# Optimization experiments

Hardware: AMD Instinct MI355X
Metric: run time of the kernel (lower is better)

The kernel has to match this reference:

```python
import jax, jax.numpy as jnp
import numpy as np

NUM_HEADS = 16
THETA = 10000.0


def _rope(x, cos, sin):
    # x: [B, H, S, d_k]; cos/sin: [S, d_k//2] broadcast over B, H
    x1 = x[..., 0::2]
    x2 = x[..., 1::2]
    r1 = cos * x1 - sin * x2
    r2 = sin * x1 + cos * x2
    # interleave back: (..., half_d, 2) -> (..., d_k)
    return jnp.stack((r1, r2), axis=-1).reshape(x.shape)


def setup_inputs() -> dict:
    key = jax.random.key(0)
    ks = jax.random.split(key, 5)
    B, S, D = 4, 2048, 1024
    scale = D ** -0.5
    x = jax.random.normal(ks[0], (B, S, D), dtype=jnp.float32)
    wq = jax.random.normal(ks[1], (D, D), dtype=jnp.float32) * scale
    wk = jax.random.normal(ks[2], (D, D), dtype=jnp.float32) * scale
    wv = jax.random.normal(ks[3], (D, D), dtype=jnp.float32) * scale
    wo = jax.random.normal(ks[4], (D, D), dtype=jnp.float32) * scale
    return {"x": x, "wq": wq, "wk": wk, "wv": wv, "wo": wo}


def reference(x, wq, wk, wv, wo):
    B, S, D = x.shape
    H = NUM_HEADS
    dk = D // H

    def proj(w):
        # x @ w.T, split heads -> [B, H, S, dk]
        y = jnp.einsum('bsd,ed->bse', x, w)
        return y.reshape(B, S, H, dk).transpose(0, 2, 1, 3)

    q, k, v = proj(wq), proj(wk), proj(wv)

    # RoPE (interleaved pairs), positions = arange(S)
    inv_freq = THETA ** (-(jnp.arange(0, dk, 2, dtype=jnp.float32) / dk))
    ang = jnp.arange(S, dtype=jnp.float32)[:, None] * inv_freq  # [S, dk//2]
    cos, sin = jnp.cos(ang), jnp.sin(ang)
    q = _rope(q, cos, sin)
    k = _rope(k, cos, sin)

    scores = jnp.einsum('bhqd,bhkd->bhqk', q, k) / jnp.sqrt(jnp.asarray(dk, x.dtype))
    causal = jnp.tril(jnp.ones((S, S), dtype=bool))  # keep self + past
    scores = jnp.where(causal, scores, -jnp.inf)
    p = jax.nn.softmax(scores, axis=-1)
    attn = jnp.einsum('bhqk,bhkd->bhqd', p, v)
    attn = attn.transpose(0, 2, 1, 3).reshape(B, S, D)
    return jnp.einsum('bsd,ed->bse', attn, wo)
```

## Files before the change

### kernel.cpp

```cpp
#include <hip/hip_runtime.h>
#include <hip/hip_bf16.h>
#include <cstdint>
#include <cstddef>

#define Bb 4
#define Ss 2048
#define Dd 1024
#define Hh 16
#define Mm (Bb*Ss)

typedef __bf16 bf16_t;
typedef __bf16 bf16x8 __attribute__((ext_vector_type(8)));
typedef __bf16 bf16x4 __attribute__((ext_vector_type(4)));
typedef float  f32x4  __attribute__((ext_vector_type(4)));
typedef float  f32x16 __attribute__((ext_vector_type(16)));
typedef unsigned int u32x4 __attribute__((ext_vector_type(4)));
typedef unsigned int u32x2 __attribute__((ext_vector_type(2)));

#define MFMA16(a,b,c) __builtin_amdgcn_mfma_f32_16x16x32_bf16(a,b,c,0,0,0)
#define MFMA32(a,b,c) __builtin_amdgcn_mfma_f32_32x32x16_bf16(a,b,c,0,0,0)

#define QSCALE 0.18033688011112042f

static __device__ __forceinline__ float fexp2(float x) {
#if __has_builtin(__builtin_amdgcn_exp2f)
  return __builtin_amdgcn_exp2f(x);
#else
  return exp2f(x);
#endif
}

static __device__ __forceinline__ bf16x8 ld16g(const bf16_t* p) {
  return __builtin_bit_cast(bf16x8, *reinterpret_cast<const u32x4*>(p));
}

static __device__ __forceinline__ void gload_lds16(const bf16_t* g, bf16_t* l) {
  __builtin_amdgcn_global_load_lds(
      (__attribute__((address_space(1))) void*)(g),
      (__attribute__((address_space(3))) void*)(l),
      16, 0, 0);
}

__global__ void prep_k(const float* __restrict__ x,  const float* __restrict__ wq,
                       const float* __restrict__ wk, const float* __restrict__ wv,
                       const float* __restrict__ wo,
                       bf16_t* __restrict__ xb, bf16_t* __restrict__ wqkv,
                       float2* __restrict__ tab) {
  int bid = blockIdx.x;
  if (bid < 8192) {
    int i = (bid * 256 + threadIdx.x) * 4;
    float4 f = *reinterpret_cast<const float4*>(x + i);
    xb[i + 0] = (bf16_t)f.x; xb[i + 1] = (bf16_t)f.y;
    xb[i + 2] = (bf16_t)f.z; xb[i + 3] = (bf16_t)f.w;
  } else if (bid < 12288) {
    int b2 = bid - 8192;
    int seg = b2 >> 10, local = b2 & 1023;
    const float* w = (seg == 0) ? wq : (seg == 1) ? wk : (seg == 2) ? wv : wo;
    int i = (local * 256 + threadIdx.x) * 4;
    float4 f = *reinterpret_cast<const float4*>(w + i);
    bf16_t* o = wqkv + (size_t)seg * (Dd * Dd) + i;
    o[0] = (bf16_t)f.x; o[1] = (bf16_t)f.y; o[2] = (bf16_t)f.z; o[3] = (bf16_t)f.w;
  } else {
    int idx = (bid - 12288) * 256 + threadIdx.x;
    int i = idx & 31, s = idx >> 5;
    float inv_freq = exp2f(-(float)i * (13.2877123795494f / 32.0f));
    float ang = (float)s * inv_freq;
    float sn, cs;
    sincosf(ang, &sn, &cs);
    tab[idx] = make_float2(cs, sn);
  }
}

template <typename OutT>
__global__ __launch_bounds__(256, 3) void gemm_r3(const bf16_t* __restrict__ A,
                                                  const bf16_t* __restrict__ Bm,
                                                  OutT* __restrict__ C0,
                                                  OutT* __restrict__ C1,
                                                  bf16_t* __restrict__ VtOut,
                                                  const float2* __restrict__ tab,
                                                  int Kdim) {
  __shared__ bf16_t As[3][128 * 32];
  __shared__ bf16_t Bs[3][128 * 32];
  const int t = threadIdx.x;
  const int lane = t & 63, w = t >> 6;
  const int l15 = lane & 15, lg = lane >> 4;
  const int wr = w >> 1, wc = w & 1;
  const int m0 = blockIdx.x * 128, n0 = blockIdx.y * 128;

  const bf16_t* gA[2];
  const bf16_t* gB[2];
#pragma unroll
  for (int i = 0; i < 2; ++i) {
    int q = i * 256 + t, row = q >> 2, sl = (q & 3) ^ ((row >> 1) & 3);
    gA[i] = A  + (size_t)(m0 + row) * Kdim + sl * 8;
    gB[i] = Bm + (size_t)(n0 + row) * Kdim + sl * 8;
  }
  const int wb = w * 64 * 8;

  auto stage = [&](int slot, int k0) {
#pragma unroll
    for (int i = 0; i < 2; ++i) {
      gload_lds16(gA[i] + k0, &As[slot][i * 2048 + wb]);
      gload_lds16(gB[i] + k0, &Bs[slot][i * 2048 + wb]);
    }
  };

  int aoff[4], boff[4];
#pragma unroll
  for (int i = 0; i < 4; ++i) {
    int row = wr * 64 + i * 16 + l15;
    aoff[i] = row * 32 + ((lg ^ ((row >> 1) & 3)) * 8);
  }
#pragma unroll
  for (int j = 0; j < 4; ++j) {
    int row = wc * 64 + j * 16 + l15;
    boff[j] = row * 32 + ((lg ^ ((row >> 1) & 3)) * 8);
  }

  f32x4 acc[4][4] = {};
  const int KT = Kdim / 32;

  stage(0, 0);
  stage(1, 32);
  for (int j = 0; j < KT; ++j) {
    if (j == KT - 1) {
      asm volatile("s_waitcnt vmcnt(0) lgkmcnt(0)" ::: "memory");
    } else {
      asm volatile("s_waitcnt vmcnt(4) lgkmcnt(0)" ::: "memory");
    }
    __builtin_amdgcn_s_barrier();
    if (j + 2 < KT) stage((j + 2) % 3, (j + 2) * 32);
    const bf16_t* ab = As[j % 3];
    const bf16_t* bb = Bs[j % 3];
    bf16x8 a[4], b[4];
#pragma unroll
    for (int jj = 0; jj < 4; ++jj)
      b[jj] = __builtin_bit_cast(bf16x8,
               *reinterpret_cast<const u32x4*>(bb + boff[jj]));
#pragma unroll
    for (int i = 0; i < 4; ++i)
      a[i] = __builtin_bit_cast(bf16x8,
               *reinterpret_cast<const u32x4*>(ab + aoff[i]));
    __builtin_amdgcn_s_setprio(1);
#pragma unroll
    for (int i = 0; i < 4; ++i)
#pragma unroll
      for (int jj = 0; jj < 4; ++jj)
        acc[i][jj] = MFMA16(a[i], b[jj], acc[i][jj]);
    __builtin_amdgcn_s_setprio(0);
  }

  const int nb = n0 & 1023;
  if (VtOut != nullptr && n0 >= 2048) {
#pragma unroll
    for (int i = 0; i < 4; ++i) {
      int rowb = m0 + wr * 64 + i * 16 + lg * 4;
      int b = rowb >> 11, s = rowb & 2047;
#pragma unroll
      for (int j = 0; j < 4; ++j) {
        int col = nb + wc * 64 + j * 16 + l15;
        int h = col >> 6, d = col & 63;
        bf16x4 ov;
#pragma unroll
        for (int r = 0; r < 4; ++r) ov[r] = (bf16_t)acc[i][j][r];
        *reinterpret_cast<u32x2*>(
            &VtOut[(((size_t)(b * 16 + h)) * 64 + d) * 2048 + s]) =
            __builtin_bit_cast(u32x2, ov);
      }
    }
    return;
  }
  OutT* Cs = (n0 < 1024) ? C0 : C1;
  const bool doRope = (tab != nullptr) && (n0 < 2048);
  const float qs = (n0 < 1024) ? QSCALE : 1.0f;

  if (doRope) {
#pragma unroll
    for (int i = 0; i < 4; ++i) {
      int rowb = m0 + wr * 64 + i * 16 + lg * 4;
#pragma unroll
      for (int j = 0; j < 4; ++j) {
        int col = nb + wc * 64 + j * 16 + l15;
        int i0 = (col & 63) >> 1;
        const bool ev = !(col & 1);
#pragma unroll
        for (int r = 0; r < 4; ++r) {
          float v = acc[i][j][r];
          float px = __shfl_xor(v, 1);
          int s = (rowb + r) & (Ss - 1);
          float2 f = tab[s * 32 + i0];
          float sn = ev ? -f.y : f.y;
          Cs[(size_t)(rowb + r) * 1024 + col] = (OutT)((f.x * v + sn * px) * qs);
        }
      }
    }
  } else {
#pragma unroll
    for (int i = 0; i < 4; ++i) {
      int rowb = m0 + wr * 64 + i * 16 + lg * 4;
#pragma unroll
      for (int j = 0; j < 4; ++j) {
        int col = nb + wc * 64 + j * 16 + l15;
#pragma unroll
        for (int r = 0; r < 4; ++r)
          Cs[(size_t)(rowb + r) * 1024 + col] = (OutT)acc[i][j][r];
      }
    }
  }
}

__global__ __launch_bounds__(256, 2) void attn_k(const bf16_t* __restrict__ Q,
                                                 const bf16_t* __restrict__ K,
                                                 const bf16_t* __restrict__ Vt,
                                                 bf16_t* __restrict__ O) {
  __shared__ bf16_t Ks[2][8192];
  __shared__ bf16_t Vs[2][8192];
  const int t = threadIdx.x, lane = t & 63, w = t >> 6;
  const int l31 = lane & 31, hi = lane >> 5, hi8 = hi * 8;
  const int bh = blockIdx.y, b = bh >> 4, h = bh & 15;
  const int bx = blockIdx.x;
  const int i = bx * 4 + w;
  const int q0a = 32 * i, q0b = 2016 - 32 * i;
  const int dtA = q0a >> 6, hfA = (q0a >> 5) & 1;
  const int dtB = q0b >> 6, hfB = (q0b >> 5) & 1;
  const int NT2 = 16 - bx;
  const bf16_t* qb = Q + (size_t)b * Ss * Dd + h * 64;
  const bf16_t* kb = K + (size_t)b * Ss * Dd + h * 64;
  const bf16_t* vtb = Vt + (size_t)bh * 64 * Ss;

  const int a_ = l31 >> 2, c_ = l31 & 3;
  const int tau = (a_ >> 1) + 2 * (a_ & 1) + ((a_ & 4) >> 1);
  const int sig = c_ + 4 * tau;

  int kfoff[4];
#pragma unroll
  for (int c = 0; c < 4; ++c) {
    int j = sig >> 1, u = (sig & 1) * 8 + c * 2 + hi;
    kfoff[c] = j * 128 + ((u ^ j) * 8);
  }
  int vfoff[2][2];
#pragma unroll
  for (int db = 0; db < 2; ++db)
#pragma unroll
    for (int ks = 0; ks < 2; ++ks) {
      int d = db * 32 + l31, j = d >> 2, u = (d & 3) * 4 + ks * 2 + hi;
      vfoff[db][ks] = j * 128 + ((u ^ j) * 8);
    }

  const int sj = t >> 4, ss = t & 15, su = ss ^ sj;
  const bf16_t* ksrc0 = kb + (size_t)(2 * sj + (su >> 3)) * Dd + (su & 7) * 8;
  const bf16_t* vsrc0 = vtb + (size_t)(4 * sj + (su >> 2)) * Ss + (su & 3) * 8;

  auto stage128 = [&](int buf, int kb0) {
    bf16_t* kd = &Ks[buf][w * 512];
    bf16_t* vd = &Vs[buf][w * 512];
#pragma unroll
    for (int st = 0; st < 4; ++st) {
      gload_lds16(ksrc0 + (size_t)(kb0 + 32 * st) * Dd, kd + st * 2048);
      gload_lds16(vsrc0 + kb0 + 32 * st,                vd + st * 2048);
    }
  };

  bf16x8 qf[2][4];
#pragma unroll
  for (int c = 0; c < 4; ++c) {
    qf[0][c] = ld16g(qb + (size_t)(q0a + l31) * Dd + c * 16 + hi8);
    qf[1][c] = ld16g(qb + (size_t)(q0b + l31) * Dd + c * 16 + hi8);
  }

  float l_[2] = {0.f, 0.f};
  f32x16 o_[2][2] = {};

  auto chain = [&](int kt, int dt, int hf, bf16x8 (&qc)[4],
                   f32x16& o0, f32x16& o1, float& lc,
                   bf16x8 (&kf)[2][4], bf16x8 (&vf)[2][2][2]) {
    if (kt > dt) return;
    const bool last = (kt == dt);
    const bool do1 = !(last && hf == 0);
    f32x16 s0 = {}, s1 = {};
    __builtin_amdgcn_s_setprio(1);
    s0 = MFMA32(kf[0][0], qc[0], s0);
    s0 = MFMA32(kf[0][1], qc[1], s0);
    s0 = MFMA32(kf[0][2], qc[2], s0);
    s0 = MFMA32(kf[0][3], qc[3], s0);
    if (do1) {
      s1 = MFMA32(kf[1][0], qc[0], s1);
      s1 = MFMA32(kf[1][1], qc[1], s1);
      s1 = MFMA32(kf[1][2], qc[2], s1);
      s1 = MFMA32(kf[1][3], qc[3], s1);
    }
    __builtin_amdgcn_s_setprio(0);
    if (last) {
      if (hf) {
#pragma unroll
        for (int reg = 0; reg < 16; ++reg) {
          const int koff = (reg & 3) + 4 * (reg >> 2) + 8 * ((reg >> 2) >> 1) + hi8;
          s1[reg] = (koff <= l31) ? s1[reg] : -INFINITY;
        }
      } else {
#pragma unroll
        for (int reg = 0; reg < 16; ++reg) {
          const int koff = (reg & 3) + 4 * (reg >> 2) + 8 * ((reg >> 2) >> 1) + hi8;
          s0[reg] = (koff <= l31) ? s0[reg] : -INFINITY;
        }
      }
    }
    float p0[16], p1[16];
#pragma unroll
    for (int r = 0; r < 16; ++r) p0[r] = fexp2(s0[r]);
    bf16x8 pa0, pa1, pb0, pb1;
#pragma unroll
    for (int r = 0; r < 8; ++r) { pa0[r] = (bf16_t)p0[r]; pa1[r] = (bf16_t)p0[r + 8]; }
    if (do1) {
#pragma unroll
      for (int r = 0; r < 16; ++r) p1[r] = fexp2(s1[r]);
#pragma unroll
      for (int r = 0; r < 8; ++r) { pb0[r] = (bf16_t)p1[r]; pb1[r] = (bf16_t)p1[r + 8]; }
#pragma unroll
      for (int r = 0; r < 16; ++r) p0[r] += p1[r];
    }
#pragma unroll
    for (int st2 = 8; st2 > 0; st2 >>= 1)
#pragma unroll
      for (int r = 0; r < st2; ++r) p0[r] += p0[r + st2];
    lc += p0[0];
    __builtin_amdgcn_s_setprio(1);
    o0 = MFMA32(vf[0][0][0], pa0, o0);
    o0 = MFMA32(vf[0][0][1], pa1, o0);
    o1 = MFMA32(vf[0][1][0], pa0, o1);
    o1 = MFMA32(vf[0][1][1], pa1, o1);
    if (do1) {
      o0 = MFMA32(vf[1][0][0], pb0, o0);
      o0 = MFMA32(vf[1][0][1], pb1, o0);
      o1 = MFMA32(vf[1][1][0], pb0, o1);
      o1 = MFMA32(vf[1][1][1], pb1, o1);
    }
    __builtin_amdgcn_s_setprio(0);
  };

  stage128(0, 0);
  for (int jj = 0; jj < NT2; ++jj) {
    asm volatile("s_waitcnt vmcnt(0) lgkmcnt(0)" ::: "memory");
    __builtin_amdgcn_s_barrier();
    if (jj + 1 < NT2) stage128((jj + 1) & 1, (jj + 1) * 128);
    const bf16_t* kbuf = &Ks[jj & 1][0];
    const bf16_t* vbuf = &Vs[jj & 1][0];
#pragma unroll
    for (int half = 0; half < 2; ++half) {
      const int kt = 2 * jj + half;
      const int base = half * 4096;
      bf16x8 kf[2][4], vf[2][2][2];
#pragma unroll
      for (int st = 0; st < 2; ++st)
#pragma unroll
        for (int c = 0; c < 4; ++c)
          kf[st][c] = __builtin_bit_cast(bf16x8,
              *reinterpret_cast<const u32x4*>(kbuf + base + st * 2048 + kfoff[c]));
#pragma unroll
      for (int st = 0; st < 2; ++st)
#pragma unroll
        for (int db = 0; db < 2; ++db)
#pragma unroll
          for (int ks = 0; ks < 2; ++ks)
            vf[st][db][ks] = __builtin_bit_cast(bf16x8,
                *reinterpret_cast<const u32x4*>(vbuf + base + st * 2048 + vfoff[db][ks]));
      chain(kt, dtA, hfA, qf[0], o_[0][0], o_[0][1], l_[0], kf, vf);
      chain(kt, dtB, hfB, qf[1], o_[1][0], o_[1][1], l_[1], kf, vf);
    }
  }

#pragma unroll
  for (int ch = 0; ch < 2; ++ch) {
    const float ltot = l_[ch] + __shfl_xor(l_[ch], 32);
    const float inv = 1.0f / ltot;
    const size_t rowoff = ((size_t)b * Ss + (ch ? q0b : q0a) + l31) * Dd + h * 64;
#pragma unroll
    for (int db = 0; db < 2; ++db)
#pragma unroll
      for (int tt = 0; tt < 4; ++tt) {
        bf16x4 ov;
#pragma unroll
        for (int c = 0; c < 4; ++c) ov[c] = (bf16_t)(o_[ch][db][4 * tt + c] * inv);
        *reinterpret_cast<u32x2*>(&O[rowoff + db * 32 + 8 * tt + 4 * hi]) =
            __builtin_bit_cast(u32x2, ov);
      }
  }
}

extern "C" void kernel_launch(void* const* d_in, const int* in_sizes, int n_in,
                              void* d_out, int out_size, void* d_ws, size_t ws_size,
                              hipStream_t stream) {
  (void)in_sizes; (void)n_in; (void)out_size; (void)ws_size;
  const float* x  = (const float*)d_in[0];
  const float* wq = (const float*)d_in[1];
  const float* wk = (const float*)d_in[2];
  const float* wv = (const float*)d_in[3];
  const float* wo = (const float*)d_in[4];
  float* out = (float*)d_out;

  char* ws = (char*)d_ws;
  const size_t MB16 = 16u << 20;
  bf16_t* xb   = (bf16_t*)(ws + 0);
  bf16_t* Qb   = (bf16_t*)(ws + 1 * MB16);
  bf16_t* Kb   = (bf16_t*)(ws + 2 * MB16);
  bf16_t* Vt   = (bf16_t*)(ws + 3 * MB16);
  bf16_t* wqkv = (bf16_t*)(ws + 4 * MB16);
  bf16_t* wob  = wqkv + 3u * Dd * Dd;
  float2* tab  = (float2*)(ws + 4 * MB16 + (8u << 20));
  bf16_t* AOb  = xb;

  prep_k<<<12544, 256, 0, stream>>>(x, wq, wk, wv, wo, xb, wqkv, tab);

  gemm_r3<bf16_t><<<dim3(Mm / 128, 24), 256, 0, stream>>>(xb, wqkv, Qb, Kb, Vt,
                                                          tab, Dd);

  attn_k<<<dim3(8, Bb * Hh), 256, 0, stream>>>(Qb, Kb, Vt, AOb);

  gemm_r3<float><<<dim3(Mm / 128, 8), 256, 0, stream>>>(AOb, wob, out, out,
                                                        nullptr, nullptr, Dd);
}
```

Before: 164.8 us.

## Use 256x256 tile, 1024-thread GEMM for fused QKV projection

Adds a new QKV projection kernel that uses 256x256 output tiles, 16 waves per block, and double-buffered LDS staging, replacing the 128x128 triple-buffered kernel for that GEMM. The larger tile raises arithmetic intensity and cuts global reloads of A and B across the grid. In exchange there are fewer blocks (384), a shallower pipeline, and a full barrier every K step across 16 waves, which could hurt latency hiding and occupancy. The old kernel is specialized to the fp32 output projection only, with the RoPE and Vt epilogues removed.

New measurement: 175.1 us. 6.2% more time.

```diff
diff --git a/kernel.cpp b/kernel.cpp
--- a/kernel.cpp
+++ b/kernel.cpp
@@ -71,13 +71,117 @@
   }
 }
 
-template <typename OutT>
+__global__ __launch_bounds__(1024, 4) void gemm_big(const bf16_t* __restrict__ A,
+                                                    const bf16_t* __restrict__ Bm,
+                                                    bf16_t* __restrict__ C0,
+                                                    bf16_t* __restrict__ C1,
+                                                    bf16_t* __restrict__ VtOut,
+                                                    const float2* __restrict__ tab,
+                                                    int Kdim) {
+  __shared__ bf16_t As[2][256 * 32];
+  __shared__ bf16_t Bs[2][256 * 32];
+  const int t = threadIdx.x;
+  const int lane = t & 63, w = t >> 6;
+  const int l15 = lane & 15, lg = lane >> 4;
+  const int wm = w >> 2, wn = w & 3;
+  const int m0 = blockIdx.x * 256, n0 = blockIdx.y * 256;
+
+  const int row_ = t >> 2, sl_ = (t & 3) ^ ((row_ >> 1) & 3);
+  const bf16_t* gA = A  + (size_t)(m0 + row_) * Kdim + sl_ * 8;
+  const bf16_t* gB = Bm + (size_t)(n0 + row_) * Kdim + sl_ * 8;
+  const int wb = w * 512;
+
+  auto stage = [&](int buf, int k0) {
+    gload_lds16(gA + k0, &As[buf][wb]);
+    gload_lds16(gB + k0, &Bs[buf][wb]);
+  };
+
+  int aoff[4], boff[4];
+#pragma unroll
+  for (int i = 0; i < 4; ++i) {
+    int row = wm * 64 + i * 16 + l15;
+    aoff[i] = row * 32 + ((lg ^ ((row >> 1) & 3)) * 8);
+  }
+#pragma unroll
+  for (int j = 0; j < 4; ++j) {
+    int row = wn * 64 + j * 16 + l15;
+    boff[j] = row * 32 + ((lg ^ ((row >> 1) & 3)) * 8);
+  }
+
+  f32x4 acc[4][4] = {};
+  const int KT = Kdim / 32;
+
+  stage(0, 0);
+  for (int j = 0; j < KT; ++j) {
+    asm volatile("s_waitcnt vmcnt(0) lgkmcnt(0)" ::: "memory");
+    __builtin_amdgcn_s_barrier();
+    if (j + 1 < KT) stage((j + 1) & 1, (j + 1) * 32);
+    const bf16_t* ab = As[j & 1];
+    const bf16_t* bb = Bs[j & 1];
+    bf16x8 a[4], b[4];
+#pragma unroll
+    for (int jj = 0; jj < 4; ++jj)
+      b[jj] = __builtin_bit_cast(bf16x8,
+               *reinterpret_cast<const u32x4*>(bb + boff[jj]));
+#pragma unroll
+    for (int i = 0; i < 4; ++i)
+      a[i] = __builtin_bit_cast(bf16x8,
+               *reinterpret_cast<const u32x4*>(ab + aoff[i]));
+    __builtin_amdgcn_s_setprio(1);
+#pragma unroll
+    for (int i = 0; i < 4; ++i)
+#pragma unroll
+      for (int jj = 0; jj < 4; ++jj)
+        acc[i][jj] = MFMA16(a[i], b[jj], acc[i][jj]);
+    __builtin_amdgcn_s_setprio(0);
+  }
+
+  const int nb = n0 & 1023;
+  if (VtOut != nullptr && n0 >= 2048) {
+#pragma unroll
+    for (int i = 0; i < 4; ++i) {
+      int rowb = m0 + wm * 64 + i * 16 + lg * 4;
+      int b = rowb >> 11, s = rowb & 2047;
+#pragma unroll
+      for (int j = 0; j < 4; ++j) {
+        int col = nb + wn * 64 + j * 16 + l15;
+        int h = col >> 6, d = col & 63;
+        bf16x4 ov;
+#pragma unroll
+        for (int r = 0; r < 4; ++r) ov[r] = (bf16_t)acc[i][j][r];
+        *reinterpret_cast<u32x2*>(
+            &VtOut[(((size_t)(b * 16 + h)) * 64 + d) * 2048 + s]) =
+            __builtin_bit_cast(u32x2, ov);
+      }
+    }
+    return;
+  }
+  bf16_t* Cs = (n0 < 1024) ? C0 : C1;
+  const float qs = (n0 < 1024) ? QSCALE : 1.0f;
+#pragma unroll
+  for (int i = 0; i < 4; ++i) {
+    int rowb = m0 + wm * 64 + i * 16 + lg * 4;
+#pragma unroll
+    for (int j = 0; j < 4; ++j) {
+      int col = nb + wn * 64 + j * 16 + l15;
+      int i0 = (col & 63) >> 1;
+      const bool ev = !(col & 1);
+#pragma unroll
+      for (int r = 0; r < 4; ++r) {
+        float v = acc[i][j][r];
+        float px = __shfl_xor(v, 1);
+        int s = (rowb + r) & (Ss - 1);
+        float2 f = tab[s * 32 + i0];
+        float sn = ev ? -f.y : f.y;
+        Cs[(size_t)(rowb + r) * 1024 + col] = (bf16_t)((f.x * v + sn * px) * qs);
+      }
+    }
+  }
+}
+
 __global__ __launch_bounds__(256, 3) void gemm_r3(const bf16_t* __restrict__ A,
                                                   const bf16_t* __restrict__ Bm,
-                                                  OutT* __restrict__ C0,
-                                                  OutT* __restrict__ C1,
-                                                  bf16_t* __restrict__ VtOut,
-                                                  const float2* __restrict__ tab,
+                                                  float* __restrict__ C0,
                                                   int Kdim) {
   __shared__ bf16_t As[3][128 * 32];
   __shared__ bf16_t Bs[3][128 * 32];
@@ -150,61 +254,15 @@
     __builtin_amdgcn_s_setprio(0);
   }
 
-  const int nb = n0 & 1023;
-  if (VtOut != nullptr && n0 >= 2048) {
-#pragma unroll
-    for (int i = 0; i < 4; ++i) {
-      int rowb = m0 + wr * 64 + i * 16 + lg * 4;
-      int b = rowb >> 11, s = rowb & 2047;
-#pragma unroll
-      for (int j = 0; j < 4; ++j) {
-        int col = nb + wc * 64 + j * 16 + l15;
-        int h = col >> 6, d = col & 63;
-        bf16x4 ov;
-#pragma unroll
-        for (int r = 0; r < 4; ++r) ov[r] = (bf16_t)acc[i][j][r];
-        *reinterpret_cast<u32x2*>(
-            &VtOut[(((size_t)(b * 16 + h)) * 64 + d) * 2048 + s]) =
-            __builtin_bit_cast(u32x2, ov);
-      }
-    }
-    return;
-  }
-  OutT* Cs = (n0 < 1024) ? C0 : C1;
-  const bool doRope = (tab != nullptr) && (n0 < 2048);
-  const float qs = (n0 < 1024) ? QSCALE : 1.0f;
-
-  if (doRope) {
-#pragma unroll
-    for (int i = 0; i < 4; ++i) {
-      int rowb = m0 + wr * 64 + i * 16 + lg * 4;
-#pragma unroll
-      for (int j = 0; j < 4; ++j) {
-        int col = nb + wc * 64 + j * 16 + l15;
-        int i0 = (col & 63) >> 1;
-        const bool ev = !(col & 1);
-#pragma unroll
-        for (int r = 0; r < 4; ++r) {
-          float v = acc[i][j][r];
-          float px = __shfl_xor(v, 1);
-          int s = (rowb + r) & (Ss - 1);
-          float2 f = tab[s * 32 + i0];
-          float sn = ev ? -f.y : f.y;
-          Cs[(size_t)(rowb + r) * 1024 + col] = (OutT)((f.x * v + sn * px) * qs);
-        }
-      }
-    }
-  } else {
-#pragma unroll
-    for (int i = 0; i < 4; ++i) {
-      int rowb = m0 + wr * 64 + i * 16 + lg * 4;
-#pragma unroll
-      for (int j = 0; j < 4; ++j) {
-        int col = nb + wc * 64 + j * 16 + l15;
-#pragma unroll
-        for (int r = 0; r < 4; ++r)
-          Cs[(size_t)(rowb + r) * 1024 + col] = (OutT)acc[i][j][r];
-      }
+#pragma unroll
+  for (int i = 0; i < 4; ++i) {
+    int rowb = m0 + wr * 64 + i * 16 + lg * 4;
+#pragma unroll
+    for (int j = 0; j < 4; ++j) {
+      int col = n0 + wc * 64 + j * 16 + l15;
+#pragma unroll
+      for (int r = 0; r < 4; ++r)
+        C0[(size_t)(rowb + r) * 1024 + col] = acc[i][j][r];
     }
   }
 }
@@ -411,11 +469,10 @@
 
   prep_k<<<12544, 256, 0, stream>>>(x, wq, wk, wv, wo, xb, wqkv, tab);
 
-  gemm_r3<bf16_t><<<dim3(Mm / 128, 24), 256, 0, stream>>>(xb, wqkv, Qb, Kb, Vt,
-                                                          tab, Dd);
+  gemm_big<<<dim3(Mm / 256, 12), 1024, 0, stream>>>(xb, wqkv, Qb, Kb, Vt,
+                                                    tab, Dd);
 
   attn_k<<<dim3(8, Bb * Hh), 256, 0, stream>>>(Qb, Kb, Vt, AOb);
 
-  gemm_r3<float><<<dim3(Mm / 128, 8), 256, 0, stream>>>(AOb, wob, out, out,
-                                                        nullptr, nullptr, Dd);
-}
+  gemm_r3<<<dim3(Mm / 128, 8), 256, 0, stream>>>(AOb, wob, out, Dd);
+}
```
